# Performance work log

Hardware: AMD Instinct MI355X
Metric: run time of the kernel (lower is better)

## Reference

```python
import jax, jax.numpy as jnp
import numpy as np

C = 256
CK = C // 8  # query/key channels = 32


def setup_inputs() -> dict:
    key = jax.random.key(0)
    ks = jax.random.split(key, 7)
    sc = 0.05
    x = jax.random.normal(ks[0], (4, C, 64, 64), dtype=jnp.float32)
    Wq = jax.random.normal(ks[1], (CK, C), dtype=jnp.float32) * sc
    bq = jax.random.normal(ks[2], (CK,), dtype=jnp.float32) * sc
    Wk = jax.random.normal(ks[3], (CK, C), dtype=jnp.float32) * sc
    bk = jax.random.normal(ks[4], (CK,), dtype=jnp.float32) * sc
    Wv = jax.random.normal(ks[5], (C, C), dtype=jnp.float32) * sc
    bv = jax.random.normal(ks[6], (C,), dtype=jnp.float32) * sc
    gamma = jnp.array([0.5], dtype=jnp.float32)  # nonzero so output/grads are nontrivial
    return {"x": x, "Wq": Wq, "bq": bq, "Wk": Wk, "bk": bk, "Wv": Wv, "bv": bv, "gamma": gamma}


def reference(x, Wq, bq, Wk, bk, Wv, bv, gamma):
    B, Cc, H, W = x.shape
    xf = x.reshape(B, Cc, H * W)  # [B, C, N]
    # 1x1 conv1d == channel-wise matmul
    f = jnp.einsum('kc,bcn->bkn', Wq, xf) + bq[None, :, None]  # [B, CK, N]
    g = jnp.einsum('kc,bcn->bkn', Wk, xf) + bk[None, :, None]  # [B, CK, N]
    h = jnp.einsum('oc,bcn->bon', Wv, xf) + bv[None, :, None]  # [B, C, N]
    # unscaled attention scores: s[b,i,j] = sum_k f[b,k,i] g[b,k,j]
    s = jnp.einsum('bki,bkj->bij', f, g)  # [B, N, N]
    beta = jax.nn.softmax(s, axis=1)      # softmax over query-side axis i (dim=1)
    o = jnp.einsum('bci,bij->bcj', h, beta)  # [B, C, N]
    o = gamma[0] * o
    return o.reshape(B, Cc, H, W)
```

## Files before the change

### kernel.cpp

```cpp
#include <hip/hip_runtime.h>
#include <math.h>

#define BB 4
#define CC 256
#define CKK 32
#define NN 4096
#define TI 32
#define NT (NN / TI)
#define NQ (NT / 4)
#define FQS (4 * 2 * 512)
#define HQS (4 * 16 * 512)
#define SM_OFF 40.0f

typedef __attribute__((ext_vector_type(8))) short short8v;
typedef __attribute__((ext_vector_type(4))) short short4v;
typedef __attribute__((ext_vector_type(4))) float f32x4;

static __device__ inline unsigned short f2bf(float x) {
    union { float f; unsigned u; } v; v.f = x;
    unsigned r = v.u + 0x7fffu + ((v.u >> 16) & 1u);
    return (unsigned short)(r >> 16);
}
static __device__ inline float bf2f(unsigned short h) {
    union { unsigned u; float f; } v; v.u = ((unsigned)h) << 16;
    return v.f;
}

__global__ __launch_bounds__(256) void prep_w(
    const float* __restrict__ Wq, const float* __restrict__ Wk,
    const float* __restrict__ Wv, unsigned short* __restrict__ Wbf)
{
    int o = blockIdx.x * 256 + threadIdx.x;
    int rb   = o >> 12;
    int rem  = o & 4095;
    int k    = rem >> 9;
    int lane = (rem >> 3) & 63;
    int e    = rem & 7;
    int row  = rb * 16 + (lane & 15);
    int c    = k * 32 + (lane >> 4) * 8 + e;
    float v;
    if (row < 32)      v = Wq[row * 256 + c];
    else if (row < 64) v = Wk[(row - 32) * 256 + c];
    else               v = Wv[(row - 64) * 256 + c];
    Wbf[o] = f2bf(v);
}

__global__ __launch_bounds__(256, 4) void proj_kernel(
    const float* __restrict__ x,
    const unsigned short* __restrict__ Wbf,
    const float* __restrict__ bq, const float* __restrict__ bk,
    const float* __restrict__ bv,
    unsigned short* __restrict__ fF, unsigned short* __restrict__ gT,
    unsigned short* __restrict__ hF)
{
    __shared__ unsigned short xsh[32 * 264];
    __shared__ unsigned short xsl[32 * 264];
    __shared__ unsigned short hstg[4][256];

    const int t = threadIdx.x;
    const int b = blockIdx.x >> 7;
    const int n_b = (blockIdx.x & 127) * 32;
    const int lane = t & 63;
    const int wave = t >> 6;
    const int jl = lane & 15;
    const int quad = lane >> 4;
    const int itb = n_b >> 5;

    {
        const int q = t & 7, cb = t >> 3;
        #pragma unroll
        for (int cc = 0; cc < 8; ++cc) {
            int c = cb + cc * 32;
            float4 v = *(const float4*)(x + ((size_t)b * CC + c) * NN + n_b + q * 4);
            float vv[4] = {v.x, v.y, v.z, v.w};
            #pragma unroll
            for (int e = 0; e < 4; ++e) {
                int n = q * 4 + e;
                unsigned short h = f2bf(vv[e]);
                unsigned short l = f2bf(vv[e] - bf2f(h));
                xsh[n * 264 + c] = h;
                xsl[n * 264 + c] = l;
            }
        }
    }
    __syncthreads();

    const int rowbase_w = wave * 80;
    #pragma unroll 1
    for (int nt = 0; nt < 2; ++nt) {
        short8v bhi[8], blo[8];
        #pragma unroll
        for (int k = 0; k < 8; ++k) {
            bhi[k] = *(const short8v*)&xsh[(nt * 16 + jl) * 264 + k * 32 + quad * 8];
            blo[k] = *(const short8v*)&xsl[(nt * 16 + jl) * 264 + k * 32 + quad * 8];
        }
        const int ng = n_b + nt * 16 + jl;
        const int ihh = (ng >> 4) & 1;
        #pragma unroll 1
        for (int mt = 0; mt < 5; ++mt) {
            int rowbase = rowbase_w + mt * 16;
            const int rb = rowbase >> 4;
            const unsigned short* wf = Wbf + (size_t)rb * 8 * 512;
            f32x4 acch = (f32x4){0.f, 0.f, 0.f, 0.f};
            f32x4 accl = (f32x4){0.f, 0.f, 0.f, 0.f};
            #pragma unroll
            for (int k = 0; k < 8; ++k) {
                short8v a = *(const short8v*)(wf + (size_t)k * 512 + lane * 8);
                acch = __builtin_amdgcn_mfma_f32_16x16x32_bf16(a, bhi[k], acch, 0, 0, 0);
                accl = __builtin_amdgcn_mfma_f32_16x16x32_bf16(a, blo[k], accl, 0, 0, 0);
            }
            f32x4 acc;
            #pragma unroll
            for (int r = 0; r < 4; ++r) acc[r] = acch[r] + accl[r];
            int rlo = rowbase + quad * 4;
            if (rowbase < 32) {
                float4 bias = *(const float4*)(bq + rlo);
                short4v o;
                o[0] = (short)f2bf(acc[0] + bias.x); o[1] = (short)f2bf(acc[1] + bias.y);
                o[2] = (short)f2bf(acc[2] + bias.z); o[3] = (short)f2bf(acc[3] + bias.w);
                size_t dst = (((size_t)b * NT + itb) * 2 + ihh) * 512
                           + (size_t)((rlo >> 3) * 16 + (ng & 15)) * 8 + (rlo & 7);
                *(short4v*)(fF + dst) = o;
            } else if (rowbase < 64) {
                float4 bias = *(const float4*)(bk + rlo - 32);
                short4v o;
                o[0] = (short)f2bf(acc[0] + bias.x); o[1] = (short)f2bf(acc[1] + bias.y);
                o[2] = (short)f2bf(acc[2] + bias.z); o[3] = (short)f2bf(acc[3] + bias.w);
                *(short4v*)(gT + ((size_t)b * NN + ng) * CKK + (rlo - 32)) = o;
            } else {
                const float* bp = bv + rlo - 64;
                const int cgh = (rowbase - 64) >> 4;
                #pragma unroll
                for (int r = 0; r < 4; ++r) {
                    int rel = ((jl >> 3) * 128) + (quad * 4 + r) * 8 + (jl & 7);
                    hstg[wave][rel] = f2bf(acc[r] + bp[r]);
                }
                short4v v = *(const short4v*)&hstg[wave][lane * 4];
                size_t hbase = (((size_t)b * NT + itb) * 16 + cgh) * 512 + nt * 256;
                *(short4v*)(hF + hbase + lane * 4) = v;
            }
        }
    }
}

__global__ __launch_bounds__(1024, 4) void attn_kernel(
    const unsigned short* __restrict__ fF,
    const unsigned short* __restrict__ gT,
    const unsigned short* __restrict__ hF,
    const float* __restrict__ gamma,
    float* __restrict__ out)
{
    __shared__ unsigned short pa[2][4][4][512];
    __shared__ float ls[8][4][16];
    __shared__ float ls2[4][16];

    const int t = threadIdx.x;
    const int lane = t & 63;
    const int wave = t >> 6;
    const int bi = blockIdx.x;
    const int b  = bi & 3;
    const int j0 = (bi >> 2) * 64;
    const int jl = lane & 15;
    const int quad = lane >> 4;

    const unsigned short* fFb = fF + (size_t)b * NT * 2 * 512;
    const unsigned short* hFb = hF + (size_t)b * NT * 16 * 512;

    const f32x4 zoff = (f32x4){-SM_OFF, -SM_OFF, -SM_OFF, -SM_OFF};

    if (wave < 8) {
        const int sub = wave >> 1;
        const int ihp = wave & 1;
        const int Lw = ((ihp * 2 + (quad >> 1)) * 16 + jl) * 8 + (quad & 1) * 4;

        short8v bg0 = *(const short8v*)(gT + ((size_t)b * NN + j0 + 0 * 16 + jl) * CKK + quad * 8);
        short8v bg1 = *(const short8v*)(gT + ((size_t)b * NN + j0 + 1 * 16 + jl) * CKK + quad * 8);
        short8v bg2 = *(const short8v*)(gT + ((size_t)b * NN + j0 + 2 * 16 + jl) * CKK + quad * 8);
        short8v bg3 = *(const short8v*)(gT + ((size_t)b * NN + j0 + 3 * 16 + jl) * CKK + quad * 8);

        float l0 = 0.f, l1 = 0.f, l2 = 0.f, l3 = 0.f;

        const unsigned short* fp = fFb + (size_t)(sub * 2 + ihp) * 512 + (size_t)lane * 8;

        #define PRODUCE(AF, PB)                                                           \
        {                                                                                 \
            f32x4 s0 = __builtin_amdgcn_mfma_f32_16x16x32_bf16(AF, bg0, zoff, 0, 0, 0);   \
            f32x4 s1 = __builtin_amdgcn_mfma_f32_16x16x32_bf16(AF, bg1, zoff, 0, 0, 0);   \
            f32x4 s2 = __builtin_amdgcn_mfma_f32_16x16x32_bf16(AF, bg2, zoff, 0, 0, 0);   \
            f32x4 s3 = __builtin_amdgcn_mfma_f32_16x16x32_bf16(AF, bg3, zoff, 0, 0, 0);   \
            float e0, e1, e2, e3; unsigned p01, p23; uint2 pw;                            \
            e0 = __expf(s0[0]); e1 = __expf(s0[1]); e2 = __expf(s0[2]); e3 = __expf(s0[3]);\
            l0 += (e0 + e1) + (e2 + e3);                                                  \
            asm("v_cvt_pk_bf16_f32 %0, %1, %2" : "=v"(p01) : "v"(e0), "v"(e1));           \
            asm("v_cvt_pk_bf16_f32 %0, %1, %2" : "=v"(p23) : "v"(e2), "v"(e3));           \
            pw.x = p01; pw.y = p23; *(uint2*)&pa[PB][sub][0][Lw] = pw;                    \
            e0 = __expf(s1[0]); e1 = __expf(s1[1]); e2 = __expf(s1[2]); e3 = __expf(s1[3]);\
            l1 += (e0 + e1) + (e2 + e3);                                                  \
            asm("v_cvt_pk_bf16_f32 %0, %1, %2" : "=v"(p01) : "v"(e0), "v"(e1));           \
            asm("v_cvt_pk_bf16_f32 %0, %1, %2" : "=v"(p23) : "v"(e2), "v"(e3));           \
            pw.x = p01; pw.y = p23; *(uint2*)&pa[PB][sub][1][Lw] = pw;                    \
            e0 = __expf(s2[0]); e1 = __expf(s2[1]); e2 = __expf(s2[2]); e3 = __expf(s2[3]);\
            l2 += (e0 + e1) + (e2 + e3);                                                  \
            asm("v_cvt_pk_bf16_f32 %0, %1, %2" : "=v"(p01) : "v"(e0), "v"(e1));           \
            asm("v_cvt_pk_bf16_f32 %0, %1, %2" : "=v"(p23) : "v"(e2), "v"(e3));           \
            pw.x = p01; pw.y = p23; *(uint2*)&pa[PB][sub][2][Lw] = pw;                    \
            e0 = __expf(s3[0]); e1 = __expf(s3[1]); e2 = __expf(s3[2]); e3 = __expf(s3[3]);\
            l3 += (e0 + e1) + (e2 + e3);                                                  \
            asm("v_cvt_pk_bf16_f32 %0, %1, %2" : "=v"(p01) : "v"(e0), "v"(e1));           \
            asm("v_cvt_pk_bf16_f32 %0, %1, %2" : "=v"(p23) : "v"(e2), "v"(e3));           \
            pw.x = p01; pw.y = p23; *(uint2*)&pa[PB][sub][3][Lw] = pw;                    \
        }

        short8v afA = *(const short8v*)fp; fp += FQS;
        short8v afB = *(const short8v*)fp; fp += FQS;
        PRODUCE(afA, 0)
        asm volatile("s_waitcnt lgkmcnt(0)" ::: "memory");
        __builtin_amdgcn_s_barrier();
        asm volatile("" ::: "memory");

        #pragma unroll 1
        for (int q = 0; q < NQ; q += 2) {
            PRODUCE(afB, 1)
            if (q + 2 < NQ) { afA = *(const short8v*)fp; fp += FQS; }
            asm volatile("s_waitcnt lgkmcnt(0)" ::: "memory");
            __builtin_amdgcn_s_barrier();
            asm volatile("" ::: "memory");

            if (q + 2 < NQ) {
                PRODUCE(afA, 0)
                if (q + 3 < NQ) { afB = *(const short8v*)fp; fp += FQS; }
            }
            asm volatile("s_waitcnt lgkmcnt(0)" ::: "memory");
            __builtin_amdgcn_s_barrier();
            asm volatile("" ::: "memory");
        }
        #undef PRODUCE

        l0 += __shfl_xor(l0, 16, 64); l0 += __shfl_xor(l0, 32, 64);
        l1 += __shfl_xor(l1, 16, 64); l1 += __shfl_xor(l1, 32, 64);
        l2 += __shfl_xor(l2, 16, 64); l2 += __shfl_xor(l2, 32, 64);
        l3 += __shfl_xor(l3, 16, 64); l3 += __shfl_xor(l3, 32, 64);
        if (quad == 0) {
            ls[wave][0][jl] = l0; ls[wave][1][jl] = l1;
            ls[wave][2][jl] = l2; ls[wave][3][jl] = l3;
        }
        __syncthreads();
        if (wave < 4 && quad == 0) {
            const int jc = wave;
            float s = ((ls[0][jc][jl] + ls[1][jc][jl]) + (ls[2][jc][jl] + ls[3][jc][jl]))
                    + ((ls[4][jc][jl] + ls[5][jc][jl]) + (ls[6][jc][jl] + ls[7][jc][jl]));
            ls2[jc][jl] = gamma[0] / s;
        }
        __syncthreads();
    } else {
        const int cw = wave - 8;
        const int cg0 = cw * 2;

        f32x4 acc[8];
        #pragma unroll
        for (int q = 0; q < 8; ++q) acc[q] = (f32x4){0.f, 0.f, 0.f, 0.f};

        const unsigned short* hq = hFb + (size_t)cg0 * 512 + (size_t)lane * 8;

        #define HLOAD(D0,D1,D2,D3,D4,D5,D6,D7, P)                      \
            D0 = *(const short8v*)(P + 0 * 8192 + 0 * 512);            \
            D1 = *(const short8v*)(P + 0 * 8192 + 1 * 512);            \
            D2 = *(const short8v*)(P + 1 * 8192 + 0 * 512);            \
            D3 = *(const short8v*)(P + 1 * 8192 + 1 * 512);            \
            D4 = *(const short8v*)(P + 2 * 8192 + 0 * 512);            \
            D5 = *(const short8v*)(P + 2 * 8192 + 1 * 512);            \
            D6 = *(const short8v*)(P + 3 * 8192 + 0 * 512);            \
            D7 = *(const short8v*)(P + 3 * 8192 + 1 * 512);

        #define PV(H0,H1,H2,H3,H4,H5,H6,H7, PB)                                                     \
        {                                                                                           \
            __builtin_amdgcn_s_setprio(1);                                                          \
            _Pragma("unroll")                                                                       \
            for (int jc2 = 0; jc2 < 4; ++jc2) {                                                     \
                short8v bp0 = *(const short8v*)&pa[PB][0][jc2][lane * 8];                           \
                acc[jc2 * 2 + 0] = __builtin_amdgcn_mfma_f32_16x16x32_bf16(H0, bp0, acc[jc2 * 2 + 0], 0, 0, 0); \
                acc[jc2 * 2 + 1] = __builtin_amdgcn_mfma_f32_16x16x32_bf16(H1, bp0, acc[jc2 * 2 + 1], 0, 0, 0); \
                short8v bp1 = *(const short8v*)&pa[PB][1][jc2][lane * 8];                           \
                acc[jc2 * 2 + 0] = __builtin_amdgcn_mfma_f32_16x16x32_bf16(H2, bp1, acc[jc2 * 2 + 0], 0, 0, 0); \
                acc[jc2 * 2 + 1] = __builtin_amdgcn_mfma_f32_16x16x32_bf16(H3, bp1, acc[jc2 * 2 + 1], 0, 0, 0); \
                short8v bp2 = *(const short8v*)&pa[PB][2][jc2][lane * 8];                           \
                acc[jc2 * 2 + 0] = __builtin_amdgcn_mfma_f32_16x16x32_bf16(H4, bp2, acc[jc2 * 2 + 0], 0, 0, 0); \
                acc[jc2 * 2 + 1] = __builtin_amdgcn_mfma_f32_16x16x32_bf16(H5, bp2, acc[jc2 * 2 + 1], 0, 0, 0); \
                short8v bp3 = *(const short8v*)&pa[PB][3][jc2][lane * 8];                           \
                acc[jc2 * 2 + 0] = __builtin_amdgcn_mfma_f32_16x16x32_bf16(H6, bp3, acc[jc2 * 2 + 0], 0, 0, 0); \
                acc[jc2 * 2 + 1] = __builtin_amdgcn_mfma_f32_16x16x32_bf16(H7, bp3, acc[jc2 * 2 + 1], 0, 0, 0); \
            }                                                                                       \
            __builtin_amdgcn_s_setprio(0);                                                          \
        }

        short8v hA0, hA1, hA2, hA3, hA4, hA5, hA6, hA7;
        short8v hB0, hB1, hB2, hB3, hB4, hB5, hB6, hB7;

        HLOAD(hA0,hA1,hA2,hA3,hA4,hA5,hA6,hA7, hq)  hq += HQS;
        HLOAD(hB0,hB1,hB2,hB3,hB4,hB5,hB6,hB7, hq)  hq += HQS;
        asm volatile("s_waitcnt lgkmcnt(0)" ::: "memory");
        __builtin_amdgcn_s_barrier();
        asm volatile("" ::: "memory");

        #pragma unroll 1
        for (int q = 0; q < NQ; q += 2) {
            PV(hA0,hA1,hA2,hA3,hA4,hA5,hA6,hA7, 0)
            if (q + 2 < NQ) { HLOAD(hA0,hA1,hA2,hA3,hA4,hA5,hA6,hA7, hq)  hq += HQS; }
            asm volatile("s_waitcnt lgkmcnt(0)" ::: "memory");
            __builtin_amdgcn_s_barrier();
            asm volatile("" ::: "memory");

            PV(hB0,hB1,hB2,hB3,hB4,hB5,hB6,hB7, 1)
            if (q + 3 < NQ) { HLOAD(hB0,hB1,hB2,hB3,hB4,hB5,hB6,hB7, hq)  hq += HQS; }
            asm volatile("s_waitcnt lgkmcnt(0)" ::: "memory");
            __builtin_amdgcn_s_barrier();
            asm volatile("" ::: "memory");
        }
        #undef HLOAD
        #undef PV

        __syncthreads();
        __syncthreads();

        #pragma unroll
        for (int jc2 = 0; jc2 < 4; ++jc2) {
            float sc = ls2[jc2][jl];
            #pragma unroll
            for (int cc = 0; cc < 2; ++cc) {
                f32x4 a = acc[jc2 * 2 + cc];
                size_t addr = ((size_t)b * CC + cw * 32 + cc * 16 + quad * 4) * NN + j0 + jc2 * 16 + jl;
                #pragma unroll
                for (int r = 0; r < 4; ++r)
                    out[addr + (size_t)r * NN] = a[r] * sc;
            }
        }
    }
}

extern "C" void kernel_launch(void* const* d_in, const int* in_sizes, int n_in,
                              void* d_out, int out_size, void* d_ws, size_t ws_size,
                              hipStream_t stream) {
    const float* x     = (const float*)d_in[0];
    const float* Wq    = (const float*)d_in[1];
    const float* bq    = (const float*)d_in[2];
    const float* Wk    = (const float*)d_in[3];
    const float* bk    = (const float*)d_in[4];
    const float* Wv    = (const float*)d_in[5];
    const float* bv    = (const float*)d_in[6];
    const float* gamma = (const float*)d_in[7];
    float* out = (float*)d_out;

    unsigned short* Wbf = (unsigned short*)d_ws;
    unsigned short* fF  = Wbf + 320 * 256;
    unsigned short* gT  = fF + (size_t)BB * NN * CKK;
    unsigned short* hF  = gT + (size_t)BB * NN * CKK;

    prep_w<<<320, 256, 0, stream>>>(Wq, Wk, Wv, Wbf);
    proj_kernel<<<BB * (NN / 32), 256, 0, stream>>>(x, Wbf, bq, bk, bv, fF, gT, hF);
    attn_kernel<<<BB * (NN / 64), 1024, 0, stream>>>(fF, gT, hF, gamma, out);
}
```

Measured before the change: 136.1 us.

## Widen attention j-tile to 128 and split output channels across two blocks

Each attention block now covers 128 key columns instead of 64 and only half of the output channels, using 8 producer waves and 4 consumer waves (768 threads). The aim is to raise the ratio of P·V MFMA work to softmax work per score tile and to make better use of each P tile in LDS. The cost is that both channel halves recompute the exponentials (QK^T plus softmax is duplicated across the pair of blocks), that accumulator registers per consumer wave double, and that occupancy drops to 3 blocks.

```diff
diff --git a/kernel.cpp b/kernel.cpp
--- a/kernel.cpp
+++ b/kernel.cpp
@@ -143,23 +143,25 @@
     }
 }
 
-__global__ __launch_bounds__(1024, 4) void attn_kernel(
+__global__ __launch_bounds__(768, 3) void attn_kernel(
     const unsigned short* __restrict__ fF,
     const unsigned short* __restrict__ gT,
     const unsigned short* __restrict__ hF,
     const float* __restrict__ gamma,
     float* __restrict__ out)
 {
-    __shared__ unsigned short pa[2][4][4][512];
-    __shared__ float ls[8][4][16];
-    __shared__ float ls2[4][16];
+    __shared__ unsigned short pa[2][4][8][512];
+    __shared__ float ls[8][8][16];
+    __shared__ float ls2[8][16];
 
     const int t = threadIdx.x;
     const int lane = t & 63;
     const int wave = t >> 6;
     const int bi = blockIdx.x;
     const int b  = bi & 3;
-    const int j0 = (bi >> 2) * 64;
+    const int u  = bi >> 2;
+    const int ch = u & 1;
+    const int j0 = (u >> 1) * 128;
     const int jl = lane & 15;
     const int quad = lane >> 4;
 
@@ -177,38 +179,40 @@
         short8v bg1 = *(const short8v*)(gT + ((size_t)b * NN + j0 + 1 * 16 + jl) * CKK + quad * 8);
         short8v bg2 = *(const short8v*)(gT + ((size_t)b * NN + j0 + 2 * 16 + jl) * CKK + quad * 8);
         short8v bg3 = *(const short8v*)(gT + ((size_t)b * NN + j0 + 3 * 16 + jl) * CKK + quad * 8);
+        short8v bg4 = *(const short8v*)(gT + ((size_t)b * NN + j0 + 4 * 16 + jl) * CKK + quad * 8);
+        short8v bg5 = *(const short8v*)(gT + ((size_t)b * NN + j0 + 5 * 16 + jl) * CKK + quad * 8);
+        short8v bg6 = *(const short8v*)(gT + ((size_t)b * NN + j0 + 6 * 16 + jl) * CKK + quad * 8);
+        short8v bg7 = *(const short8v*)(gT + ((size_t)b * NN + j0 + 7 * 16 + jl) * CKK + quad * 8);
 
         float l0 = 0.f, l1 = 0.f, l2 = 0.f, l3 = 0.f;
+        float l4 = 0.f, l5 = 0.f, l6 = 0.f, l7 = 0.f;
 
         const unsigned short* fp = fFb + (size_t)(sub * 2 + ihp) * 512 + (size_t)lane * 8;
 
-        #define PRODUCE(AF, PB)                                                           \
-        {                                                                                 \
-            f32x4 s0 = __builtin_amdgcn_mfma_f32_16x16x32_bf16(AF, bg0, zoff, 0, 0, 0);   \
-            f32x4 s1 = __builtin_amdgcn_mfma_f32_16x16x32_bf16(AF, bg1, zoff, 0, 0, 0);   \
-            f32x4 s2 = __builtin_amdgcn_mfma_f32_16x16x32_bf16(AF, bg2, zoff, 0, 0, 0);   \
-            f32x4 s3 = __builtin_amdgcn_mfma_f32_16x16x32_bf16(AF, bg3, zoff, 0, 0, 0);   \
-            float e0, e1, e2, e3; unsigned p01, p23; uint2 pw;                            \
-            e0 = __expf(s0[0]); e1 = __expf(s0[1]); e2 = __expf(s0[2]); e3 = __expf(s0[3]);\
-            l0 += (e0 + e1) + (e2 + e3);                                                  \
-            asm("v_cvt_pk_bf16_f32 %0, %1, %2" : "=v"(p01) : "v"(e0), "v"(e1));           \
-            asm("v_cvt_pk_bf16_f32 %0, %1, %2" : "=v"(p23) : "v"(e2), "v"(e3));           \
-            pw.x = p01; pw.y = p23; *(uint2*)&pa[PB][sub][0][Lw] = pw;                    \
-            e0 = __expf(s1[0]); e1 = __expf(s1[1]); e2 = __expf(s1[2]); e3 = __expf(s1[3]);\
-            l1 += (e0 + e1) + (e2 + e3);                                                  \
-            asm("v_cvt_pk_bf16_f32 %0, %1, %2" : "=v"(p01) : "v"(e0), "v"(e1));           \
-            asm("v_cvt_pk_bf16_f32 %0, %1, %2" : "=v"(p23) : "v"(e2), "v"(e3));           \
-            pw.x = p01; pw.y = p23; *(uint2*)&pa[PB][sub][1][Lw] = pw;                    \
-            e0 = __expf(s2[0]); e1 = __expf(s2[1]); e2 = __expf(s2[2]); e3 = __expf(s2[3]);\
-            l2 += (e0 + e1) + (e2 + e3);                                                  \
-            asm("v_cvt_pk_bf16_f32 %0, %1, %2" : "=v"(p01) : "v"(e0), "v"(e1));           \
-            asm("v_cvt_pk_bf16_f32 %0, %1, %2" : "=v"(p23) : "v"(e2), "v"(e3));           \
-            pw.x = p01; pw.y = p23; *(uint2*)&pa[PB][sub][2][Lw] = pw;                    \
-            e0 = __expf(s3[0]); e1 = __expf(s3[1]); e2 = __expf(s3[2]); e3 = __expf(s3[3]);\
-            l3 += (e0 + e1) + (e2 + e3);                                                  \
-            asm("v_cvt_pk_bf16_f32 %0, %1, %2" : "=v"(p01) : "v"(e0), "v"(e1));           \
-            asm("v_cvt_pk_bf16_f32 %0, %1, %2" : "=v"(p23) : "v"(e2), "v"(e3));           \
-            pw.x = p01; pw.y = p23; *(uint2*)&pa[PB][sub][3][Lw] = pw;                    \
+        #define PJC(SV, LV, JC, PB)                                                        \
+        {                                                                                  \
+            float e0 = __expf(SV[0]), e1 = __expf(SV[1]);                                  \
+            float e2 = __expf(SV[2]), e3 = __expf(SV[3]);                                  \
+            LV += (e0 + e1) + (e2 + e3);                                                   \
+            unsigned p01, p23;                                                             \
+            asm("v_cvt_pk_bf16_f32 %0, %1, %2" : "=v"(p01) : "v"(e0), "v"(e1));            \
+            asm("v_cvt_pk_bf16_f32 %0, %1, %2" : "=v"(p23) : "v"(e2), "v"(e3));            \
+            uint2 pw; pw.x = p01; pw.y = p23;                                              \
+            *(uint2*)&pa[PB][sub][JC][Lw] = pw;                                            \
+        }
+
+        #define PRODUCE(AF, PB)                                                            \
+        {                                                                                  \
+            f32x4 s0 = __builtin_amdgcn_mfma_f32_16x16x32_bf16(AF, bg0, zoff, 0, 0, 0);    \
+            f32x4 s1 = __builtin_amdgcn_mfma_f32_16x16x32_bf16(AF, bg1, zoff, 0, 0, 0);    \
+            f32x4 s2 = __builtin_amdgcn_mfma_f32_16x16x32_bf16(AF, bg2, zoff, 0, 0, 0);    \
+            f32x4 s3 = __builtin_amdgcn_mfma_f32_16x16x32_bf16(AF, bg3, zoff, 0, 0, 0);    \
+            f32x4 s4 = __builtin_amdgcn_mfma_f32_16x16x32_bf16(AF, bg4, zoff, 0, 0, 0);    \
+            f32x4 s5 = __builtin_amdgcn_mfma_f32_16x16x32_bf16(AF, bg5, zoff, 0, 0, 0);    \
+            f32x4 s6 = __builtin_amdgcn_mfma_f32_16x16x32_bf16(AF, bg6, zoff, 0, 0, 0);    \
+            f32x4 s7 = __builtin_amdgcn_mfma_f32_16x16x32_bf16(AF, bg7, zoff, 0, 0, 0);    \
+            PJC(s0, l0, 0, PB) PJC(s1, l1, 1, PB) PJC(s2, l2, 2, PB) PJC(s3, l3, 3, PB)    \
+            PJC(s4, l4, 4, PB) PJC(s5, l5, 5, PB) PJC(s6, l6, 6, PB) PJC(s7, l7, 7, PB)    \
         }
 
         short8v afA = *(const short8v*)fp; fp += FQS;
@@ -235,17 +239,24 @@
             asm volatile("" ::: "memory");
         }
         #undef PRODUCE
+        #undef PJC
 
         l0 += __shfl_xor(l0, 16, 64); l0 += __shfl_xor(l0, 32, 64);
         l1 += __shfl_xor(l1, 16, 64); l1 += __shfl_xor(l1, 32, 64);
         l2 += __shfl_xor(l2, 16, 64); l2 += __shfl_xor(l2, 32, 64);
         l3 += __shfl_xor(l3, 16, 64); l3 += __shfl_xor(l3, 32, 64);
+        l4 += __shfl_xor(l4, 16, 64); l4 += __shfl_xor(l4, 32, 64);
+        l5 += __shfl_xor(l5, 16, 64); l5 += __shfl_xor(l5, 32, 64);
+        l6 += __shfl_xor(l6, 16, 64); l6 += __shfl_xor(l6, 32, 64);
+        l7 += __shfl_xor(l7, 16, 64); l7 += __shfl_xor(l7, 32, 64);
         if (quad == 0) {
             ls[wave][0][jl] = l0; ls[wave][1][jl] = l1;
             ls[wave][2][jl] = l2; ls[wave][3][jl] = l3;
+            ls[wave][4][jl] = l4; ls[wave][5][jl] = l5;
+            ls[wave][6][jl] = l6; ls[wave][7][jl] = l7;
         }
         __syncthreads();
-        if (wave < 4 && quad == 0) {
+        if (quad == 0) {
             const int jc = wave;
             float s = ((ls[0][jc][jl] + ls[1][jc][jl]) + (ls[2][jc][jl] + ls[3][jc][jl]))
                     + ((ls[4][jc][jl] + ls[5][jc][jl]) + (ls[6][jc][jl] + ls[7][jc][jl]));
@@ -254,11 +265,11 @@
         __syncthreads();
     } else {
         const int cw = wave - 8;
-        const int cg0 = cw * 2;
-
-        f32x4 acc[8];
+        const int cg0 = ch * 8 + cw * 2;
+
+        f32x4 acc[16];
         #pragma unroll
-        for (int q = 0; q < 8; ++q) acc[q] = (f32x4){0.f, 0.f, 0.f, 0.f};
+        for (int q = 0; q < 16; ++q) acc[q] = (f32x4){0.f, 0.f, 0.f, 0.f};
 
         const unsigned short* hq = hFb + (size_t)cg0 * 512 + (size_t)lane * 8;
 
@@ -272,25 +283,21 @@
             D6 = *(const short8v*)(P + 3 * 8192 + 0 * 512);            \
             D7 = *(const short8v*)(P + 3 * 8192 + 1 * 512);
 
-        #define PV(H0,H1,H2,H3,H4,H5,H6,H7, PB)                                                     \
+        #define PVT(HA, HB, S, PB)                                                                  \
         {                                                                                           \
-            __builtin_amdgcn_s_setprio(1);                                                          \
             _Pragma("unroll")                                                                       \
-            for (int jc2 = 0; jc2 < 4; ++jc2) {                                                     \
-                short8v bp0 = *(const short8v*)&pa[PB][0][jc2][lane * 8];                           \
-                acc[jc2 * 2 + 0] = __builtin_amdgcn_mfma_f32_16x16x32_bf16(H0, bp0, acc[jc2 * 2 + 0], 0, 0, 0); \
-                acc[jc2 * 2 + 1] = __builtin_amdgcn_mfma_f32_16x16x32_bf16(H1, bp0, acc[jc2 * 2 + 1], 0, 0, 0); \
-                short8v bp1 = *(const short8v*)&pa[PB][1][jc2][lane * 8];                           \
-                acc[jc2 * 2 + 0] = __builtin_amdgcn_mfma_f32_16x16x32_bf16(H2, bp1, acc[jc2 * 2 + 0], 0, 0, 0); \
-                acc[jc2 * 2 + 1] = __builtin_amdgcn_mfma_f32_16x16x32_bf16(H3, bp1, acc[jc2 * 2 + 1], 0, 0, 0); \
-                short8v bp2 = *(const short8v*)&pa[PB][2][jc2][lane * 8];                           \
-                acc[jc2 * 2 + 0] = __builtin_amdgcn_mfma_f32_16x16x32_bf16(H4, bp2, acc[jc2 * 2 + 0], 0, 0, 0); \
-                acc[jc2 * 2 + 1] = __builtin_amdgcn_mfma_f32_16x16x32_bf16(H5, bp2, acc[jc2 * 2 + 1], 0, 0, 0); \
-                short8v bp3 = *(const short8v*)&pa[PB][3][jc2][lane * 8];                           \
-                acc[jc2 * 2 + 0] = __builtin_amdgcn_mfma_f32_16x16x32_bf16(H6, bp3, acc[jc2 * 2 + 0], 0, 0, 0); \
-                acc[jc2 * 2 + 1] = __builtin_amdgcn_mfma_f32_16x16x32_bf16(H7, bp3, acc[jc2 * 2 + 1], 0, 0, 0); \
+            for (int jc2 = 0; jc2 < 8; ++jc2) {                                                     \
+                short8v bp = *(const short8v*)&pa[PB][S][jc2][lane * 8];                            \
+                acc[jc2 * 2 + 0] = __builtin_amdgcn_mfma_f32_16x16x32_bf16(HA, bp, acc[jc2 * 2 + 0], 0, 0, 0); \
+                acc[jc2 * 2 + 1] = __builtin_amdgcn_mfma_f32_16x16x32_bf16(HB, bp, acc[jc2 * 2 + 1], 0, 0, 0); \
             }                                                                                       \
-            __builtin_amdgcn_s_setprio(0);                                                          \
+        }
+        #define PV(H0,H1,H2,H3,H4,H5,H6,H7, PB)                        \
+        {                                                              \
+            __builtin_amdgcn_s_setprio(1);                             \
+            PVT(H0, H1, 0, PB) PVT(H2, H3, 1, PB)                      \
+            PVT(H4, H5, 2, PB) PVT(H6, H7, 3, PB)                      \
+            __builtin_amdgcn_s_setprio(0);                             \
         }
 
         short8v hA0, hA1, hA2, hA3, hA4, hA5, hA6, hA7;
@@ -317,18 +324,20 @@
             asm volatile("" ::: "memory");
         }
         #undef HLOAD
+        #undef PVT
         #undef PV
 
         __syncthreads();
         __syncthreads();
 
+        const int c0 = ch * 128 + cw * 32;
         #pragma unroll
-        for (int jc2 = 0; jc2 < 4; ++jc2) {
+        for (int jc2 = 0; jc2 < 8; ++jc2) {
             float sc = ls2[jc2][jl];
             #pragma unroll
             for (int cc = 0; cc < 2; ++cc) {
                 f32x4 a = acc[jc2 * 2 + cc];
-                size_t addr = ((size_t)b * CC + cw * 32 + cc * 16 + quad * 4) * NN + j0 + jc2 * 16 + jl;
+                size_t addr = ((size_t)b * CC + c0 + cc * 16 + quad * 4) * NN + j0 + jc2 * 16 + jl;
                 #pragma unroll
                 for (int r = 0; r < 4; ++r)
                     out[addr + (size_t)r * NN] = a[r] * sc;
@@ -357,5 +366,5 @@
 
     prep_w<<<320, 256, 0, stream>>>(Wq, Wk, Wv, Wbf);
     proj_kernel<<<BB * (NN / 32), 256, 0, stream>>>(x, Wbf, bq, bk, bv, fF, gT, hF);
-    attn_kernel<<<BB * (NN / 64), 1024, 0, stream>>>(fF, gT, hF, gamma, out);
-}
+    attn_kernel<<<BB * (NN / 128) * 2, 768, 0, stream>>>(fF, gT, hF, gamma, out);
+}
```

Result: slower. 142.2 us (+4.5%).
